# Optimization experiments

Hardware: AMD Instinct MI355X
Metric: run time of the kernel (lower is better)

## Reference

```python
import jax, jax.numpy as jnp
import numpy as np

B, S, D, H = 2, 2048, 1024, 16
DH = D // H
EPS = 1e-5


def _ln(x, g, b):
    m = jnp.mean(x, axis=-1, keepdims=True)
    v = jnp.mean((x - m) ** 2, axis=-1, keepdims=True)
    return (x - m) * jax.lax.rsqrt(v + EPS) * g + b


def setup_inputs() -> dict:
    key = jax.random.key(0)
    ks = jax.random.split(key, 16)
    w = lambda k, shp: jax.random.normal(k, shp, jnp.float32) * 0.02
    return {
        "x": jax.random.normal(ks[0], (B, S, D), jnp.float32),
        # semantic preprocessor: Linear(D,2D) -> ReLU -> Linear(2D,D), residual + LN
        "pW1": w(ks[1], (D, 2 * D)), "pb1": jnp.zeros((2 * D,), jnp.float32),
        "pW2": w(ks[2], (2 * D, D)), "pb2": jnp.zeros((D,), jnp.float32),
        "gp": jnp.ones((D,), jnp.float32), "bp": jnp.zeros((D,), jnp.float32),
        # multi-head attention projections
        "Wq": w(ks[3], (D, D)), "bq": jnp.zeros((D,), jnp.float32),
        "Wk": w(ks[4], (D, D)), "bk": jnp.zeros((D,), jnp.float32),
        "Wv": w(ks[5], (D, D)), "bv": jnp.zeros((D,), jnp.float32),
        "Wo": w(ks[6], (D, D)), "bo": jnp.zeros((D,), jnp.float32),
        "g1": jnp.ones((D,), jnp.float32), "b1": jnp.zeros((D,), jnp.float32),
        # FFN: Linear(D,4D) -> ReLU -> Linear(4D,D)
        "Wf1": w(ks[7], (D, 4 * D)), "bf1": jnp.zeros((4 * D,), jnp.float32),
        "Wf2": w(ks[8], (4 * D, D)), "bf2": jnp.zeros((D,), jnp.float32),
        "g2": jnp.ones((D,), jnp.float32), "b2": jnp.zeros((D,), jnp.float32),
    }


def reference(x, pW1, pb1, pW2, pb2, gp, bp,
              Wq, bq, Wk, bk, Wv, bv, Wo, bo, g1, b1,
              Wf1, bf1, Wf2, bf2, g2, b2):
    # specialized 'semantic' preprocessor (dropout = identity in eval)
    h = jax.nn.relu(x @ pW1 + pb1) @ pW2 + pb2
    s = _ln(x + h, gp, bp)                       # [B,S,D]
    # naive multi-head attention
    q = (s @ Wq + bq).reshape(B, S, H, DH)
    k = (s @ Wk + bk).reshape(B, S, H, DH)
    v = (s @ Wv + bv).reshape(B, S, H, DH)
    scores = jnp.einsum("bqhd,bkhd->bhqk", q, k) / np.sqrt(DH).astype(np.float32)
    attn = jax.nn.softmax(scores, axis=-1)       # [B,H,S,S]
    ctx = jnp.einsum("bhqk,bkhd->bqhd", attn, v).reshape(B, S, D)
    attn_out = ctx @ Wo + bo
    y = _ln(s + attn_out, g1, b1)
    # FFN (dropouts = identity)
    f = jax.nn.relu(y @ Wf1 + bf1) @ Wf2 + bf2
    return _ln(y + f, g2, b2)
```

## Files before the change

kernel.cpp:

```cpp
#include <hip/hip_runtime.h>
#include <cstdint>
#include <cstddef>

typedef _Float16 f16;
typedef _Float16 f16x8 __attribute__((ext_vector_type(8)));
typedef _Float16 f16x4 __attribute__((ext_vector_type(4)));
typedef float    f32x4 __attribute__((ext_vector_type(4)));
typedef float    f32x16 __attribute__((ext_vector_type(16)));
typedef unsigned int uint2v __attribute__((ext_vector_type(2)));

#define MFMA16(a,b,c) __builtin_amdgcn_mfma_f32_16x16x32_f16(a, b, c, 0, 0, 0)
#define MFMA32(a,b,c) __builtin_amdgcn_mfma_f32_32x32x16_f16(a, b, c, 0, 0, 0)

static __device__ __forceinline__ void gload_lds16(const void* g, void* l) {
  __builtin_amdgcn_global_load_lds(
      (const __attribute__((address_space(1))) unsigned int*)g,
      (__attribute__((address_space(3))) unsigned int*)l, 16, 0, 0);
}

static __device__ __forceinline__ int pkh(float a, float b) {
  auto t = __builtin_amdgcn_cvt_pkrtz(a, b);
  return __builtin_bit_cast(int, t);
}

static __device__ __forceinline__ float ex2(float x) {
  return __builtin_amdgcn_exp2f(x);
}

static __device__ __forceinline__ uint2v pswap(int a, int b) {
  return __builtin_amdgcn_permlane32_swap((unsigned)a, (unsigned)b, false, false);
}
static __device__ __forceinline__ float xhalf_max(float x) {
  uint2v r = pswap(__builtin_bit_cast(int, x), __builtin_bit_cast(int, x));
  return fmaxf(__builtin_bit_cast(float, r.x), __builtin_bit_cast(float, r.y));
}
static __device__ __forceinline__ float xhalf_sum(float x) {
  uint2v r = pswap(__builtin_bit_cast(int, x), __builtin_bit_cast(int, x));
  return __builtin_bit_cast(float, r.x) + __builtin_bit_cast(float, r.y);
}

__global__ __launch_bounds__(256) void cast_kernel(const float* __restrict__ x,
                                                   f16* __restrict__ y, int n4) {
  int i = blockIdx.x * 256 + threadIdx.x;
  if (i < n4) {
    float4 v = ((const float4*)x)[i];
    f16x4 h;
    h[0] = (f16)v.x; h[1] = (f16)v.y; h[2] = (f16)v.z; h[3] = (f16)v.w;
    *(f16x4*)(y + (size_t)i * 4) = h;
  }
}

__global__ __launch_bounds__(256) void wtrans(const float* __restrict__ W,
                                              f16* __restrict__ Wt, int K, int N,
                                              float scale) {
  __shared__ float tile[32][33];
  const int n0 = blockIdx.x * 32, k0 = blockIdx.y * 32;
  const int c = threadIdx.x & 31, r = threadIdx.x >> 5;
#pragma unroll
  for (int i = 0; i < 4; i++) {
    int row = r + i * 8;
    tile[row][c] = W[(size_t)(k0 + row) * N + n0 + c];
  }
  __syncthreads();
#pragma unroll
  for (int i = 0; i < 4; i++) {
    int row = r + i * 8;
    Wt[(size_t)(n0 + row) * K + k0 + c] = (f16)(tile[c][row] * scale);
  }
}

__global__ __launch_bounds__(256) void qkvbias_kernel(const float* __restrict__ bq,
                                                      const float* __restrict__ bk,
                                                      const float* __restrict__ bv,
                                                      float* __restrict__ bqkv) {
  int i = blockIdx.x * 256 + threadIdx.x;
  if (i < 1024)       bqkv[i] = bq[i] * 0.18033688f;
  else if (i < 2048)  bqkv[i] = bk[i - 1024];
  else if (i < 3072)  bqkv[i] = bv[i - 2048];
}

template <int MODE>
__global__ __launch_bounds__(256, 2)
void gemm_kernel(const f16* __restrict__ A, const f16* __restrict__ W,
                 const float* __restrict__ bias, void* __restrict__ out,
                 f16* __restrict__ vt, int N, int K, int gx) {
  __shared__ __align__(16) f16 lsA[128 * 64];
  __shared__ __align__(16) f16 lsB[128 * 64];
  const int tid  = threadIdx.x;
  const int lane = tid & 63;
  const int wid  = tid >> 6;
  const int frow = lane & 15;
  const int kgrp = lane >> 4;
  const int wmBase = (wid >> 1) * 64;
  const int wnBase = (wid & 1) * 64;

  const int bid = blockIdx.x;
  const int xcd = bid & 7, slot = bid >> 3;
  const int bm = (xcd << 2) + slot / gx;
  const int bn = slot % gx;

  const f32x4 zero4 = {0.f, 0.f, 0.f, 0.f};
  f32x4 acc[4][4];
#pragma unroll
  for (int i = 0; i < 4; i++)
#pragma unroll
    for (int j = 0; j < 4; j++) acc[i][j] = zero4;

  const f16* aSrc[4]; int lOffA[4];
  const f16* bSrc[4]; int lOffB[4];
#pragma unroll
  for (int i = 0; i < 4; i++) {
    int c_lin = i * 256 + wid * 64 + lane;
    int row = c_lin >> 3;
    int ch  = (c_lin & 7) ^ (row & 7);
    aSrc[i] = A + (size_t)(bm * 128 + row) * K + ch * 8;
    bSrc[i] = W + (size_t)(bn * 128 + row) * K + ch * 8;
    lOffA[i] = (i * 256 + wid * 64) * 8;
    lOffB[i] = lOffA[i];
  }

  const int nk = K >> 6;
  for (int ks = 0; ks < nk; ++ks) {
#pragma unroll
    for (int i = 0; i < 4; i++) gload_lds16(aSrc[i] + ks * 64, &lsA[lOffA[i]]);
#pragma unroll
    for (int i = 0; i < 4; i++) gload_lds16(bSrc[i] + ks * 64, &lsB[lOffB[i]]);
    __syncthreads();
#pragma unroll
    for (int kk = 0; kk < 2; kk++) {
      f16x8 af[4], bf[4];
#pragma unroll
      for (int i = 0; i < 4; i++) {
        int row = wmBase + i * 16 + frow;
        af[i] = *(const f16x8*)&lsA[row * 64 + (((kk * 4 + kgrp) ^ (row & 7)) << 3)];
      }
#pragma unroll
      for (int j = 0; j < 4; j++) {
        int row = wnBase + j * 16 + frow;
        bf[j] = *(const f16x8*)&lsB[row * 64 + (((kk * 4 + kgrp) ^ (row & 7)) << 3)];
      }
#pragma unroll
      for (int i = 0; i < 4; i++)
#pragma unroll
        for (int j = 0; j < 4; j++) acc[i][j] = MFMA16(af[i], bf[j], acc[i][j]);
    }
    __syncthreads();
  }

#pragma unroll
  for (int j = 0; j < 4; j++) {
    const int col = bn * 128 + wnBase + j * 16 + frow;
    const float bb = bias[col];
#pragma unroll
    for (int i = 0; i < 4; i++) {
      const int row0 = bm * 128 + wmBase + i * 16 + kgrp * 4;
      if (MODE == 3 && col >= 2048) {
        const int vcol = col - 2048;
        const int bh = (row0 >> 11) * 16 + (vcol >> 6);
        const int d  = vcol & 63;
        const int kv = row0 & 2047;
        f16x4 pk;
#pragma unroll
        for (int r = 0; r < 4; r++) pk[r] = (f16)(acc[i][j][r] + bb);
        *(f16x4*)(vt + ((size_t)bh * 64 + d) * 2048 + kv) = pk;
      } else {
#pragma unroll
        for (int r = 0; r < 4; r++) {
          float v = acc[i][j][r] + bb;
          if (MODE == 1) v = fmaxf(v, 0.f);
          ((f16*)out)[(size_t)(row0 + r) * N + col] = (f16)v;
        }
      }
    }
  }
}

__global__ __launch_bounds__(256, 2)
void gemm_splitk(const f16* __restrict__ A, const f16* __restrict__ W,
                 f16* __restrict__ outp, int K) {
  __shared__ __align__(16) f16 lsA[128 * 64];
  __shared__ __align__(16) f16 lsB[128 * 64];
  const int tid  = threadIdx.x;
  const int lane = tid & 63;
  const int wid  = tid >> 6;
  const int frow = lane & 15;
  const int kgrp = lane >> 4;
  const int wmBase = (wid >> 1) * 64;
  const int wnBase = (wid & 1) * 64;

  const int bid = blockIdx.x;
  const int xcd = bid & 7, slot = bid >> 3;
  const int q = slot >> 3, bn = slot & 7;
  const int bmkp = xcd * 8 + q;
  const int bm = bmkp >> 1, kp = bmkp & 1;
  const int Kh = K >> 1;
  const f16* Ab = A + kp * Kh;
  const f16* Wb = W + kp * Kh;

  const f32x4 zero4 = {0.f, 0.f, 0.f, 0.f};
  f32x4 acc[4][4];
#pragma unroll
  for (int i = 0; i < 4; i++)
#pragma unroll
    for (int j = 0; j < 4; j++) acc[i][j] = zero4;

  const f16* aSrc[4]; const f16* bSrc[4]; int lOff[4];
#pragma unroll
  for (int i = 0; i < 4; i++) {
    int c_lin = i * 256 + wid * 64 + lane;
    int row = c_lin >> 3;
    int ch  = (c_lin & 7) ^ (row & 7);
    aSrc[i] = Ab + (size_t)(bm * 128 + row) * K + ch * 8;
    bSrc[i] = Wb + (size_t)(bn * 128 + row) * K + ch * 8;
    lOff[i] = (i * 256 + wid * 64) * 8;
  }

  const int nk = Kh >> 6;
  for (int ks = 0; ks < nk; ++ks) {
#pragma unroll
    for (int i = 0; i < 4; i++) gload_lds16(aSrc[i] + ks * 64, &lsA[lOff[i]]);
#pragma unroll
    for (int i = 0; i < 4; i++) gload_lds16(bSrc[i] + ks * 64, &lsB[lOff[i]]);
    __syncthreads();
#pragma unroll
    for (int kk = 0; kk < 2; kk++) {
      f16x8 af[4], bf[4];
#pragma unroll
      for (int i = 0; i < 4; i++) {
        int row = wmBase + i * 16 + frow;
        af[i] = *(const f16x8*)&lsA[row * 64 + (((kk * 4 + kgrp) ^ (row & 7)) << 3)];
      }
#pragma unroll
      for (int j = 0; j < 4; j++) {
        int row = wnBase + j * 16 + frow;
        bf[j] = *(const f16x8*)&lsB[row * 64 + (((kk * 4 + kgrp) ^ (row & 7)) << 3)];
      }
#pragma unroll
      for (int i = 0; i < 4; i++)
#pragma unroll
        for (int j = 0; j < 4; j++) acc[i][j] = MFMA16(af[i], bf[j], acc[i][j]);
    }
    __syncthreads();
  }

  f16* op = outp + (size_t)kp * 4096 * 1024;
#pragma unroll
  for (int j = 0; j < 4; j++) {
    const int col = bn * 128 + wnBase + j * 16 + frow;
#pragma unroll
    for (int i = 0; i < 4; i++) {
      const int row0 = bm * 128 + wmBase + i * 16 + kgrp * 4;
#pragma unroll
      for (int r = 0; r < 4; r++)
        op[(size_t)(row0 + r) * 1024 + col] = (f16)acc[i][j][r];
    }
  }
}

__global__ __launch_bounds__(256)
void ln_res2(const f16* __restrict__ p, const f16* __restrict__ res,
             const float* __restrict__ bias, const float* __restrict__ g,
             const float* __restrict__ be, float* __restrict__ of,
             f16* __restrict__ ob) {
  const int row = blockIdx.x, t = threadIdx.x;
  const size_t off = (size_t)row * 1024 + t * 4;
  const f16x4 a = *(const f16x4*)(p + off);
  const f16x4 b = *(const f16x4*)(p + (size_t)4096 * 1024 + off);
  const f16x4 rr = *(const f16x4*)(res + off);
  const float4 bb = ((const float4*)bias)[t];
  float v0 = (float)a[0] + (float)b[0] + bb.x + (float)rr[0];
  float v1 = (float)a[1] + (float)b[1] + bb.y + (float)rr[1];
  float v2 = (float)a[2] + (float)b[2] + bb.z + (float)rr[2];
  float v3 = (float)a[3] + (float)b[3] + bb.w + (float)rr[3];
  float s = v0 + v1 + v2 + v3;
  float q = v0 * v0 + v1 * v1 + v2 * v2 + v3 * v3;
#pragma unroll
  for (int o = 1; o < 64; o <<= 1) {
    s += __shfl_xor(s, o);
    q += __shfl_xor(q, o);
  }
  __shared__ float ss[4], sq[4];
  if ((t & 63) == 0) { ss[t >> 6] = s; sq[t >> 6] = q; }
  __syncthreads();
  s = ss[0] + ss[1] + ss[2] + ss[3];
  q = sq[0] + sq[1] + sq[2] + sq[3];
  const float mean = s * (1.f / 1024.f);
  const float var  = q * (1.f / 1024.f) - mean * mean;
  const float rstd = rsqrtf(var + 1e-5f);
  const float4 gv = ((const float4*)g)[t];
  const float4 bv = ((const float4*)be)[t];
  float4 ov;
  ov.x = (v0 - mean) * rstd * gv.x + bv.x;
  ov.y = (v1 - mean) * rstd * gv.y + bv.y;
  ov.z = (v2 - mean) * rstd * gv.z + bv.z;
  ov.w = (v3 - mean) * rstd * gv.w + bv.w;
  if (of) ((float4*)(of + (size_t)row * 1024))[t] = ov;
  if (ob) {
    f16x4 hv;
    hv[0] = (f16)ov.x; hv[1] = (f16)ov.y; hv[2] = (f16)ov.z; hv[3] = (f16)ov.w;
    *(f16x4*)(ob + off) = hv;
  }
}

__global__ __launch_bounds__(256, 4)
void attn_kernel(const f16* __restrict__ Qp, const f16* __restrict__ Kp,
                 const f16* __restrict__ Vt, f16* __restrict__ opart,
                 float* __restrict__ Lbuf, int ldq) {
  __shared__ __align__(16) f16 lsKb[2 * 64 * 64];
  __shared__ __align__(16) f16 lsVb[2 * 64 * 64];
  const int tid = threadIdx.x, lane = tid & 63, wid = tid >> 6;
  const int qcol = lane & 31;
  const int hi = lane >> 5;
  const int bid = blockIdx.x;
  const int idx = bid >> 3;
  const int bh = ((bid & 7) << 2) | (idx & 3);
  const int rest = idx >> 2;
  const int part = rest & 1;
  const int qt = rest >> 1;
  const int b = bh >> 4, h = bh & 15;
  const size_t rb = (size_t)b * 2048;
  const int hc = h * 64;
  const int kv0 = part * 1024;
  const int qrow = qt * 128 + wid * 32 + qcol;

  f16x8 qf[4];
  {
    const f16* qp = Qp + (rb + qrow) * ldq + hc;
#pragma unroll
    for (int kc = 0; kc < 4; kc++) qf[kc] = *(const f16x8*)(qp + kc * 16 + hi * 8);
  }

  f32x16 ot0, ot1;
#pragma unroll
  for (int i = 0; i < 16; i++) { ot0[i] = 0.f; ot1[i] = 0.f; }
  float mrun = -1e30f, lrun = 0.f;

  const f16 *kS0, *kS1, *vS0, *vS1;
  int off0, off1;
  {
    int c0 = wid * 64 + lane;
    int r0 = c0 >> 3, ch0 = (c0 & 7) ^ (r0 & 7);
    int c1 = 256 + wid * 64 + lane;
    int r1 = c1 >> 3, ch1 = (c1 & 7) ^ (r1 & 7);
    kS0 = Kp + (rb + kv0 + r0) * ldq + hc + ch0 * 8;
    kS1 = Kp + (rb + kv0 + r1) * ldq + hc + ch1 * 8;
    const f16* vbase = Vt + (size_t)bh * 64 * 2048 + kv0;
    vS0 = vbase + (size_t)r0 * 2048 + ch0 * 8;
    vS1 = vbase + (size_t)r1 * 2048 + ch1 * 8;
    off0 = (wid * 64) * 8;
    off1 = (256 + wid * 64) * 8;
  }

#define ASTAGE(T, PB)                                                    \
  {                                                                      \
    f16* kd = lsKb + (PB) * 4096;                                        \
    f16* vd = lsVb + (PB) * 4096;                                        \
    const size_t ko = (size_t)(T) * 64 * ldq;                            \
    const size_t vo = (size_t)(T) * 64;                                  \
    gload_lds16(kS0 + ko, kd + off0);                                    \
    gload_lds16(kS1 + ko, kd + off1);                                    \
    gload_lds16(vS0 + vo, vd + off0);                                    \
    gload_lds16(vS1 + vo, vd + off1);                                    \
  }

  ASTAGE(0, 0);
  asm volatile("s_waitcnt vmcnt(0)" ::: "memory");
  __builtin_amdgcn_s_barrier();

  for (int kt = 0; kt < 16; ++kt) {
    const int cur = kt & 1;
    if (kt < 15) ASTAGE(kt + 1, cur ^ 1);
    const f16* kb = lsKb + cur * 4096;
    const f16* vb = lsVb + cur * 4096;

    f32x16 s0, s1;
#pragma unroll
    for (int i = 0; i < 16; i++) { s0[i] = 0.f; s1[i] = 0.f; }
    const int kr0 = qcol, kr1 = 32 + qcol;
    __builtin_amdgcn_s_setprio(1);
#pragma unroll
    for (int kc = 0; kc < 4; kc++) {
      f16x8 a0 = *(const f16x8*)&kb[kr0 * 64 + (((kc * 2 + hi) ^ (kr0 & 7)) << 3)];
      f16x8 a1 = *(const f16x8*)&kb[kr1 * 64 + (((kc * 2 + hi) ^ (kr1 & 7)) << 3)];
      s0 = MFMA32(a0, qf[kc], s0);
      s1 = MFMA32(a1, qf[kc], s1);
    }
    __builtin_amdgcn_s_setprio(0);

    float mx[16];
#pragma unroll
    for (int r = 0; r < 16; r++) mx[r] = fmaxf(s0[r], s1[r]);
#pragma unroll
    for (int w = 8; w > 0; w >>= 1)
#pragma unroll
      for (int r = 0; r < w; r++) mx[r] = fmaxf(mx[r], mx[r + w]);
    float pmax = xhalf_max(mx[0]);
    if (__any(pmax > mrun + 11.54f)) {
      float mn = fmaxf(mrun, pmax);
      float fac = ex2(mrun - mn);
      mrun = mn;
      lrun *= fac;
#pragma unroll
      for (int i = 0; i < 16; i++) { ot0[i] *= fac; ot1[i] *= fac; }
    }
#pragma unroll
    for (int r = 0; r < 16; r++) {
      s0[r] = ex2(s0[r] - mrun);
      s1[r] = ex2(s1[r] - mrun);
    }
    float sm[16];
#pragma unroll
    for (int r = 0; r < 16; r++) sm[r] = s0[r] + s1[r];
#pragma unroll
    for (int w = 8; w > 0; w >>= 1)
#pragma unroll
      for (int r = 0; r < w; r++) sm[r] += sm[r + w];
    lrun += xhalf_sum(sm[0]);

#pragma unroll
    for (int st = 0; st < 2; ++st) {
#pragma unroll
      for (int c0 = 0; c0 < 2; c0++) {
        const int c8 = c0 * 8;
        int a0, a1, b0, b1;
        if (st == 0) {
          a0 = pkh(s0[c8 + 0], s0[c8 + 1]); a1 = pkh(s0[c8 + 2], s0[c8 + 3]);
          b0 = pkh(s0[c8 + 4], s0[c8 + 5]); b1 = pkh(s0[c8 + 6], s0[c8 + 7]);
        } else {
          a0 = pkh(s1[c8 + 0], s1[c8 + 1]); a1 = pkh(s1[c8 + 2], s1[c8 + 3]);
          b0 = pkh(s1[c8 + 4], s1[c8 + 5]); b1 = pkh(s1[c8 + 6], s1[c8 + 7]);
        }
        uint2v r0 = pswap(a0, b0);
        uint2v r1 = pswap(a1, b1);
        int4 wv;
        wv.x = (int)r0.x; wv.y = (int)r1.x; wv.z = (int)r0.y; wv.w = (int)r1.y;
        f16x8 pfrag = __builtin_bit_cast(f16x8, wv);
        const int ch = st * 4 + c0 * 2 + hi;
        const int vr0 = qcol, vr1 = 32 + qcol;
        f16x8 av0 = *(const f16x8*)&vb[vr0 * 64 + ((ch ^ (vr0 & 7)) << 3)];
        f16x8 av1 = *(const f16x8*)&vb[vr1 * 64 + ((ch ^ (vr1 & 7)) << 3)];
        __builtin_amdgcn_s_setprio(1);
        ot0 = MFMA32(av0, pfrag, ot0);
        ot1 = MFMA32(av1, pfrag, ot1);
        __builtin_amdgcn_s_setprio(0);
      }
    }
    asm volatile("s_waitcnt vmcnt(0)" ::: "memory");
    __builtin_amdgcn_s_barrier();
  }
#undef ASTAGE

  const float rinv = 1.f / lrun;
  const size_t pbase = ((size_t)part * 32 + bh) * 2048 + qrow;
  f16* pp = opart + pbase * 64;
#pragma unroll
  for (int rr = 0; rr < 16; rr += 2) {
    const int d = (rr & 3) + 8 * (rr >> 2) + 4 * hi;
    *(int*)(pp + d)      = pkh(ot0[rr] * rinv, ot0[rr + 1] * rinv);
    *(int*)(pp + 32 + d) = pkh(ot1[rr] * rinv, ot1[rr + 1] * rinv);
  }
  if (hi == 0) Lbuf[pbase] = mrun + __builtin_amdgcn_logf(lrun);
}

__global__ __launch_bounds__(256)
void combine_kernel(const f16* __restrict__ opart, const float* __restrict__ Lbuf,
                    f16* __restrict__ ctx) {
  const int bid = blockIdx.x;
  const int bh = bid >> 5, qblk = bid & 31;
  const int t = threadIdx.x;
  const int q = qblk * 64 + (t >> 2);
  const int dp = (t & 3) * 16;
  const size_t base = (size_t)bh * 2048 + q;
  const size_t p1o = (size_t)32 * 2048;
  const float L0 = Lbuf[base];
  const float L1 = Lbuf[p1o + base];
  const float L = fmaxf(L0, L1);
  float w0 = ex2(L0 - L), w1 = ex2(L1 - L);
  const float rs = 1.f / (w0 + w1);
  w0 *= rs; w1 *= rs;
  const f16* p0 = opart + base * 64 + dp;
  const f16* p1 = opart + (p1o + base) * 64 + dp;
  f16x8 a0 = *(const f16x8*)p0, a1 = *(const f16x8*)(p0 + 8);
  f16x8 c0 = *(const f16x8*)p1, c1 = *(const f16x8*)(p1 + 8);
  f16x8 o0, o1;
#pragma unroll
  for (int j = 0; j < 8; j++) {
    o0[j] = (f16)(w0 * (float)a0[j] + w1 * (float)c0[j]);
    o1[j] = (f16)(w0 * (float)a1[j] + w1 * (float)c1[j]);
  }
  const int b = bh >> 4, h = bh & 15;
  f16* op = ctx + ((size_t)b * 2048 + q) * 1024 + h * 64 + dp;
  *(f16x8*)op = o0;
  *(f16x8*)(op + 8) = o1;
}

extern "C" void kernel_launch(void* const* d_in, const int* in_sizes, int n_in,
                              void* d_out, int out_size, void* d_ws, size_t ws_size,
                              hipStream_t stream) {
  const float* x   = (const float*)d_in[0];
  const float* pW1 = (const float*)d_in[1];
  const float* pb1 = (const float*)d_in[2];
  const float* pW2 = (const float*)d_in[3];
  const float* pb2 = (const float*)d_in[4];
  const float* gp  = (const float*)d_in[5];
  const float* bp  = (const float*)d_in[6];
  const float* Wq  = (const float*)d_in[7];
  const float* bq  = (const float*)d_in[8];
  const float* Wk  = (const float*)d_in[9];
  const float* bk  = (const float*)d_in[10];
  const float* Wv  = (const float*)d_in[11];
  const float* bv  = (const float*)d_in[12];
  const float* Wo  = (const float*)d_in[13];
  const float* bo  = (const float*)d_in[14];
  const float* g1  = (const float*)d_in[15];
  const float* b1  = (const float*)d_in[16];
  const float* Wf1 = (const float*)d_in[17];
  const float* bf1 = (const float*)d_in[18];
  const float* Wf2 = (const float*)d_in[19];
  const float* bf2 = (const float*)d_in[20];
  const float* g2  = (const float*)d_in[21];
  const float* b2  = (const float*)d_in[22];

  char* ws = (char*)d_ws;
  const size_t MB = 1024 * 1024;
  if (ws_size < 121 * MB) return;

  f16*   wtP1 = (f16*)(ws);
  f16*   wtP2 = (f16*)(ws + 4 * MB);
  f16*   wtQ  = (f16*)(ws + 8 * MB);
  f16*   wtO  = (f16*)(ws + 14 * MB);
  f16*   wtF1 = (f16*)(ws + 16 * MB);
  f16*   wtF2 = (f16*)(ws + 24 * MB);
  f16*   big  = (f16*)(ws + 32 * MB);
  f16*   xb   = (f16*)(ws + 64 * MB);
  f16*   sb   = (f16*)(ws + 72 * MB);
  f16*   ybuf = (f16*)(ws + 80 * MB);
  f16*   ctx  = (f16*)(ws + 88 * MB);
  f16*   part = (f16*)(ws + 96 * MB);
  f16*   opart= (f16*)(ws + 96 * MB);
  float* Lbuf = (float*)(ws + 112 * MB);
  float* bqkv = (float*)(ws + 112 * MB + 512 * 1024);
  f16*   wtK  = wtQ + (size_t)1024 * 1024;
  f16*   wtV  = wtQ + (size_t)2048 * 1024;
  f16*   Vt   = big + (size_t)4096 * 3072;

  dim3 blk(256);
  qkvbias_kernel<<<12, blk, 0, stream>>>(bq, bk, bv, bqkv);
  cast_kernel<<<4096, blk, 0, stream>>>(x, xb, 1048576);
  wtrans<<<dim3(64, 32),  blk, 0, stream>>>(pW1, wtP1, 1024, 2048, 1.f);
  wtrans<<<dim3(32, 64),  blk, 0, stream>>>(pW2, wtP2, 2048, 1024, 1.f);
  wtrans<<<dim3(32, 32),  blk, 0, stream>>>(Wq,  wtQ,  1024, 1024, 0.18033688f);
  wtrans<<<dim3(32, 32),  blk, 0, stream>>>(Wk,  wtK,  1024, 1024, 1.f);
  wtrans<<<dim3(32, 32),  blk, 0, stream>>>(Wv,  wtV,  1024, 1024, 1.f);
  wtrans<<<dim3(32, 32),  blk, 0, stream>>>(Wo,  wtO,  1024, 1024, 1.f);
  wtrans<<<dim3(128, 32), blk, 0, stream>>>(Wf1, wtF1, 1024, 4096, 1.f);
  wtrans<<<dim3(32, 128), blk, 0, stream>>>(Wf2, wtF2, 4096, 1024, 1.f);

  gemm_kernel<1><<<512, blk, 0, stream>>>(xb, wtP1, pb1, big, nullptr, 2048, 1024, 16);
  gemm_splitk<<<512, blk, 0, stream>>>(big, wtP2, part, 2048);
  ln_res2<<<4096, blk, 0, stream>>>(part, xb, pb2, gp, bp, nullptr, sb);
  gemm_kernel<3><<<768, blk, 0, stream>>>(sb, wtQ, bqkv, big, Vt, 3072, 1024, 24);
  attn_kernel<<<1024, blk, 0, stream>>>(big, big + 1024, Vt, opart, Lbuf, 3072);
  combine_kernel<<<1024, blk, 0, stream>>>(opart, Lbuf, ctx);
  gemm_splitk<<<512, blk, 0, stream>>>(ctx, wtO, part, 1024);
  ln_res2<<<4096, blk, 0, stream>>>(part, sb, bo, g1, b1, nullptr, ybuf);
  gemm_kernel<1><<<1024, blk, 0, stream>>>(ybuf, wtF1, bf1, big, nullptr, 4096, 1024, 32);
  gemm_splitk<<<512, blk, 0, stream>>>(big, wtF2, part, 4096);
  ln_res2<<<4096, blk, 0, stream>>>(part, ybuf, bf2, g2, b2, (float*)d_out, nullptr);
}
```

Baseline: 288.9 us.

## Merge prep kernels into one launch and compute softmax row sum via MFMA

After: 272.3 us. 1.06x faster.

```diff
diff --git a/kernel.cpp b/kernel.cpp
--- a/kernel.cpp
+++ b/kernel.cpp
@@ -34,49 +34,75 @@
   uint2v r = pswap(__builtin_bit_cast(int, x), __builtin_bit_cast(int, x));
   return fmaxf(__builtin_bit_cast(float, r.x), __builtin_bit_cast(float, r.y));
 }
-static __device__ __forceinline__ float xhalf_sum(float x) {
-  uint2v r = pswap(__builtin_bit_cast(int, x), __builtin_bit_cast(int, x));
-  return __builtin_bit_cast(float, r.x) + __builtin_bit_cast(float, r.y);
-}
-
-__global__ __launch_bounds__(256) void cast_kernel(const float* __restrict__ x,
-                                                   f16* __restrict__ y, int n4) {
-  int i = blockIdx.x * 256 + threadIdx.x;
-  if (i < n4) {
+static __device__ __forceinline__ float f3(float a, float b, float c) {
+  return fmaxf(fmaxf(a, b), c);
+}
+
+static __device__ __forceinline__ void wtrans_blk(float (*tile)[33],
+                                                  const float* __restrict__ W,
+                                                  f16* __restrict__ Wt,
+                                                  int K, int N, int gx,
+                                                  float scale, int lb) {
+  const int n0 = (lb % gx) * 32, k0 = (lb / gx) * 32;
+  const int c = threadIdx.x & 31, r = threadIdx.x >> 5;
+#pragma unroll
+  for (int i = 0; i < 4; i++) {
+    int row = r + i * 8;
+    tile[row][c] = W[(size_t)(k0 + row) * N + n0 + c];
+  }
+  __syncthreads();
+#pragma unroll
+  for (int i = 0; i < 4; i++) {
+    int row = r + i * 8;
+    Wt[(size_t)(n0 + row) * K + k0 + c] = (f16)(tile[c][row] * scale);
+  }
+}
+
+__global__ __launch_bounds__(256)
+void prep_kernel(const float* __restrict__ x, f16* __restrict__ xb,
+                 const float* __restrict__ pW1, f16* __restrict__ wtP1,
+                 const float* __restrict__ pW2, f16* __restrict__ wtP2,
+                 const float* __restrict__ Wq,  f16* __restrict__ wtQ,
+                 const float* __restrict__ Wk,  f16* __restrict__ wtK,
+                 const float* __restrict__ Wv,  f16* __restrict__ wtV,
+                 const float* __restrict__ Wo,  f16* __restrict__ wtO,
+                 const float* __restrict__ Wf1, f16* __restrict__ wtF1,
+                 const float* __restrict__ Wf2, f16* __restrict__ wtF2,
+                 const float* __restrict__ bq, const float* __restrict__ bk,
+                 const float* __restrict__ bv, float* __restrict__ bqkv) {
+  __shared__ float tile[32][33];
+  int b = blockIdx.x;
+  if (b < 4096) {
+    int i = b * 256 + threadIdx.x;
     float4 v = ((const float4*)x)[i];
     f16x4 h;
     h[0] = (f16)v.x; h[1] = (f16)v.y; h[2] = (f16)v.z; h[3] = (f16)v.w;
-    *(f16x4*)(y + (size_t)i * 4) = h;
-  }
-}
-
-__global__ __launch_bounds__(256) void wtrans(const float* __restrict__ W,
-                                              f16* __restrict__ Wt, int K, int N,
-                                              float scale) {
-  __shared__ float tile[32][33];
-  const int n0 = blockIdx.x * 32, k0 = blockIdx.y * 32;
-  const int c = threadIdx.x & 31, r = threadIdx.x >> 5;
-#pragma unroll
-  for (int i = 0; i < 4; i++) {
-    int row = r + i * 8;
-    tile[row][c] = W[(size_t)(k0 + row) * N + n0 + c];
-  }
-  __syncthreads();
-#pragma unroll
-  for (int i = 0; i < 4; i++) {
-    int row = r + i * 8;
-    Wt[(size_t)(n0 + row) * K + k0 + c] = (f16)(tile[c][row] * scale);
-  }
-}
-
-__global__ __launch_bounds__(256) void qkvbias_kernel(const float* __restrict__ bq,
-                                                      const float* __restrict__ bk,
-                                                      const float* __restrict__ bv,
-                                                      float* __restrict__ bqkv) {
-  int i = blockIdx.x * 256 + threadIdx.x;
-  if (i < 1024)       bqkv[i] = bq[i] * 0.18033688f;
-  else if (i < 2048)  bqkv[i] = bk[i - 1024];
-  else if (i < 3072)  bqkv[i] = bv[i - 2048];
+    *(f16x4*)(xb + (size_t)i * 4) = h;
+    return;
+  }
+  b -= 4096;
+  if (b < 2048) { wtrans_blk(tile, pW1, wtP1, 1024, 2048, 64, 1.f, b); return; }
+  b -= 2048;
+  if (b < 2048) { wtrans_blk(tile, pW2, wtP2, 2048, 1024, 32, 1.f, b); return; }
+  b -= 2048;
+  if (b < 1024) { wtrans_blk(tile, Wq, wtQ, 1024, 1024, 32, 0.18033688f, b); return; }
+  b -= 1024;
+  if (b < 1024) { wtrans_blk(tile, Wk, wtK, 1024, 1024, 32, 1.f, b); return; }
+  b -= 1024;
+  if (b < 1024) { wtrans_blk(tile, Wv, wtV, 1024, 1024, 32, 1.f, b); return; }
+  b -= 1024;
+  if (b < 1024) { wtrans_blk(tile, Wo, wtO, 1024, 1024, 32, 1.f, b); return; }
+  b -= 1024;
+  if (b < 4096) { wtrans_blk(tile, Wf1, wtF1, 1024, 4096, 128, 1.f, b); return; }
+  b -= 4096;
+  if (b < 4096) { wtrans_blk(tile, Wf2, wtF2, 4096, 1024, 32, 1.f, b); return; }
+  b -= 4096;
+  {
+    int i = b * 256 + threadIdx.x;
+    if (i < 1024)       bqkv[i] = bq[i] * 0.18033688f;
+    else if (i < 2048)  bqkv[i] = bk[i - 1024];
+    else if (i < 3072)  bqkv[i] = bv[i - 2048];
+  }
 }
 
 template <int MODE>
@@ -107,7 +133,7 @@
     for (int j = 0; j < 4; j++) acc[i][j] = zero4;
 
   const f16* aSrc[4]; int lOffA[4];
-  const f16* bSrc[4]; int lOffB[4];
+  const f16* bSrc[4];
 #pragma unroll
   for (int i = 0; i < 4; i++) {
     int c_lin = i * 256 + wid * 64 + lane;
@@ -116,7 +142,6 @@
     aSrc[i] = A + (size_t)(bm * 128 + row) * K + ch * 8;
     bSrc[i] = W + (size_t)(bn * 128 + row) * K + ch * 8;
     lOffA[i] = (i * 256 + wid * 64) * 8;
-    lOffB[i] = lOffA[i];
   }
 
   const int nk = K >> 6;
@@ -124,7 +149,7 @@
 #pragma unroll
     for (int i = 0; i < 4; i++) gload_lds16(aSrc[i] + ks * 64, &lsA[lOffA[i]]);
 #pragma unroll
-    for (int i = 0; i < 4; i++) gload_lds16(bSrc[i] + ks * 64, &lsB[lOffB[i]]);
+    for (int i = 0; i < 4; i++) gload_lds16(bSrc[i] + ks * 64, &lsB[lOffA[i]]);
     __syncthreads();
 #pragma unroll
     for (int kk = 0; kk < 2; kk++) {
@@ -329,11 +354,14 @@
 #pragma unroll
     for (int kc = 0; kc < 4; kc++) qf[kc] = *(const f16x8*)(qp + kc * 16 + hi * 8);
   }
-
-  f32x16 ot0, ot1;
-#pragma unroll
-  for (int i = 0; i < 16; i++) { ot0[i] = 0.f; ot1[i] = 0.f; }
-  float mrun = -1e30f, lrun = 0.f;
+  f16x8 ones;
+#pragma unroll
+  for (int i = 0; i < 8; i++) ones[i] = (f16)1.0f;
+
+  f32x16 ot0, ot1, lacc;
+#pragma unroll
+  for (int i = 0; i < 16; i++) { ot0[i] = 0.f; ot1[i] = 0.f; lacc[i] = 0.f; }
+  float mrun = -1e30f;
 
   const f16 *kS0, *kS1, *vS0, *vS1;
   int off0, off1;
@@ -387,35 +415,34 @@
     }
     __builtin_amdgcn_s_setprio(0);
 
-    float mx[16];
-#pragma unroll
-    for (int r = 0; r < 16; r++) mx[r] = fmaxf(s0[r], s1[r]);
-#pragma unroll
-    for (int w = 8; w > 0; w >>= 1)
-#pragma unroll
-      for (int r = 0; r < w; r++) mx[r] = fmaxf(mx[r], mx[r + w]);
-    float pmax = xhalf_max(mx[0]);
+    float t10[11];
+#pragma unroll
+    for (int r = 0; r < 10; r++) {
+      float e0 = (3 * r + 0 < 16) ? s0[(3 * r + 0) & 15] : s1[(3 * r + 0) & 15];
+      float e1 = (3 * r + 1 < 16) ? s0[(3 * r + 1) & 15] : s1[(3 * r + 1) & 15];
+      float e2 = (3 * r + 2 < 16) ? s0[(3 * r + 2) & 15] : s1[(3 * r + 2) & 15];
+      t10[r] = f3(e0, e1, e2);
+    }
+    t10[10] = fmaxf(s1[14], s1[15]);
+    float p0 = f3(t10[0], t10[1], t10[2]);
+    float p1 = f3(t10[3], t10[4], t10[5]);
+    float p2 = f3(t10[6], t10[7], t10[8]);
+    float p3 = fmaxf(t10[9], t10[10]);
+    float pmax = xhalf_max(fmaxf(fmaxf(p0, p1), fmaxf(p2, p3)));
     if (__any(pmax > mrun + 11.54f)) {
       float mn = fmaxf(mrun, pmax);
       float fac = ex2(mrun - mn);
       mrun = mn;
-      lrun *= fac;
-#pragma unroll
-      for (int i = 0; i < 16; i++) { ot0[i] *= fac; ot1[i] *= fac; }
+#pragma unroll
+      for (int i = 0; i < 16; i++) {
+        ot0[i] *= fac; ot1[i] *= fac; lacc[i] *= fac;
+      }
     }
 #pragma unroll
     for (int r = 0; r < 16; r++) {
       s0[r] = ex2(s0[r] - mrun);
       s1[r] = ex2(s1[r] - mrun);
     }
-    float sm[16];
-#pragma unroll
-    for (int r = 0; r < 16; r++) sm[r] = s0[r] + s1[r];
-#pragma unroll
-    for (int w = 8; w > 0; w >>= 1)
-#pragma unroll
-      for (int r = 0; r < w; r++) sm[r] += sm[r + w];
-    lrun += xhalf_sum(sm[0]);
 
 #pragma unroll
     for (int st = 0; st < 2; ++st) {
@@ -442,6 +469,7 @@
         __builtin_amdgcn_s_setprio(1);
         ot0 = MFMA32(av0, pfrag, ot0);
         ot1 = MFMA32(av1, pfrag, ot1);
+        lacc = MFMA32(ones, pfrag, lacc);
         __builtin_amdgcn_s_setprio(0);
       }
     }
@@ -450,7 +478,8 @@
   }
 #undef ASTAGE
 
-  const float rinv = 1.f / lrun;
+  const float lfin = lacc[0];
+  const float rinv = 1.f / lfin;
   const size_t pbase = ((size_t)part * 32 + bh) * 2048 + qrow;
   f16* pp = opart + pbase * 64;
 #pragma unroll
@@ -459,7 +488,7 @@
     *(int*)(pp + d)      = pkh(ot0[rr] * rinv, ot0[rr + 1] * rinv);
     *(int*)(pp + 32 + d) = pkh(ot1[rr] * rinv, ot1[rr + 1] * rinv);
   }
-  if (hi == 0) Lbuf[pbase] = mrun + __builtin_amdgcn_logf(lrun);
+  if (hi == 0) Lbuf[pbase] = mrun + __builtin_amdgcn_logf(lfin);
 }
 
 __global__ __launch_bounds__(256)
@@ -545,16 +574,9 @@
   f16*   Vt   = big + (size_t)4096 * 3072;
 
   dim3 blk(256);
-  qkvbias_kernel<<<12, blk, 0, stream>>>(bq, bk, bv, bqkv);
-  cast_kernel<<<4096, blk, 0, stream>>>(x, xb, 1048576);
-  wtrans<<<dim3(64, 32),  blk, 0, stream>>>(pW1, wtP1, 1024, 2048, 1.f);
-  wtrans<<<dim3(32, 64),  blk, 0, stream>>>(pW2, wtP2, 2048, 1024, 1.f);
-  wtrans<<<dim3(32, 32),  blk, 0, stream>>>(Wq,  wtQ,  1024, 1024, 0.18033688f);
-  wtrans<<<dim3(32, 32),  blk, 0, stream>>>(Wk,  wtK,  1024, 1024, 1.f);
-  wtrans<<<dim3(32, 32),  blk, 0, stream>>>(Wv,  wtV,  1024, 1024, 1.f);
-  wtrans<<<dim3(32, 32),  blk, 0, stream>>>(Wo,  wtO,  1024, 1024, 1.f);
-  wtrans<<<dim3(128, 32), blk, 0, stream>>>(Wf1, wtF1, 1024, 4096, 1.f);
-  wtrans<<<dim3(32, 128), blk, 0, stream>>>(Wf2, wtF2, 4096, 1024, 1.f);
+  prep_kernel<<<20492, blk, 0, stream>>>(x, xb, pW1, wtP1, pW2, wtP2,
+                                         Wq, wtQ, Wk, wtK, Wv, wtV, Wo, wtO,
+                                         Wf1, wtF1, Wf2, wtF2, bq, bk, bv, bqkv);
 
   gemm_kernel<1><<<512, blk, 0, stream>>>(xb, wtP1, pb1, big, nullptr, 2048, 1024, 16);
   gemm_splitk<<<512, blk, 0, stream>>>(big, wtP2, part, 2048);
```
